# Kernel tuning notes

Hardware: AMD Instinct MI355X
Metric: run time of the kernel (lower is better)

Reference implementation:

```python
import jax, jax.numpy as jnp
import numpy as np

B, S, D, F, E = 4, 1024, 768, 3072, 8
TOP_K = 2


def setup_inputs() -> dict:
    key = jax.random.key(0)
    k0, k1, k2, k3 = jax.random.split(key, 4)
    x = jax.random.normal(k0, (B, S, D), dtype=jnp.float32)
    w_router = jax.random.normal(k1, (D, E), dtype=jnp.float32) * 0.02
    w1 = jax.random.normal(k2, (E, D, F), dtype=jnp.float32) * 0.02
    b1 = jnp.zeros((E, F), dtype=jnp.float32)
    w2 = jax.random.normal(k3, (E, F, D), dtype=jnp.float32) * 0.02
    b2 = jnp.zeros((E, D), dtype=jnp.float32)
    return {"x": x, "w_router": w_router, "w1": w1, "b1": b1, "w2": w2, "b2": b2}


def reference(x, w_router, w1, b1, w2, b2):
    # Router: logits [B,S,E] -> softmax -> top-k -> renormalize
    router_logits = jnp.einsum('bsd,de->bse', x, w_router)
    router_probs = jax.nn.softmax(router_logits, axis=-1)
    top_k_probs, top_k_idx = jax.lax.top_k(router_probs, TOP_K)  # [B,S,K]
    top_k_probs = top_k_probs / (jnp.sum(top_k_probs, axis=-1, keepdims=True) + 1e-8)
    # Combine weights [B,S,E]: weight for expert e if selected, else 0.
    # (top-k indices are distinct, so summing one-hots over k is exact.)
    combine = jnp.sum(
        jax.nn.one_hot(top_k_idx, E, dtype=x.dtype) * top_k_probs[..., None], axis=-2)
    # Dense per-expert FFN over ALL tokens (faithful to the original masked-dense math).
    h = jax.nn.gelu(jnp.einsum('bsd,edf->ebsf', x, w1) + b1[:, None, None, :],
                    approximate=False)  # [E,B,S,F]
    expert_out = jnp.einsum('ebsf,efd->ebsd', h, w2) + b2[:, None, None, :]  # [E,B,S,D]
    output = jnp.einsum('ebsd,bse->bsd', expert_out, combine)
    return output
```

## Files before the change

### kernel.cpp

```cpp
#include <hip/hip_runtime.h>
#include <math.h>

typedef __bf16 bf16x8 __attribute__((ext_vector_type(8)));
typedef float f32x4 __attribute__((ext_vector_type(4)));

#define B_ 4
#define S_ 1024
#define D_ 768
#define F_ 3072
#define E_ 8
#define NTOK 4096
#define NSLOTP 9216

__device__ __forceinline__ void gload_lds16(const void* g, void* s) {
  __builtin_amdgcn_global_load_lds((const __attribute__((address_space(1))) void*)g,
                                   (__attribute__((address_space(3))) void*)s, 16, 0, 0);
}

template<int N> __device__ __forceinline__ void wait_vmcnt() {
  if constexpr (N == 0)      asm volatile("s_waitcnt vmcnt(0)" ::: "memory");
  else if constexpr (N == 6) asm volatile("s_waitcnt vmcnt(6)" ::: "memory");
  else static_assert(N == 0, "unhandled vmcnt");
}
#define BAR()    asm volatile("s_barrier" ::: "memory")
#define LGKM0()  do { asm volatile("s_waitcnt lgkmcnt(0)" ::: "memory"); \
                      __builtin_amdgcn_sched_barrier(0); } while (0)

__device__ __forceinline__ float gelu_f(float v) {
  float u = v * (0.7978845608f + 0.0356774081f * v * v);
  float t = 1.f - 2.f / (1.f + __expf(2.f * u));
  return 0.5f * v * (1.f + t);
}

__global__ __launch_bounds__(256) void k_router(const float* __restrict__ x,
    const float* __restrict__ wr, int* __restrict__ tki, float* __restrict__ tkw) {
  int wid = threadIdx.x >> 6, lane = threadIdx.x & 63;
  int t = blockIdx.x * 4 + wid;
  const float* xp = x + (size_t)t * D_;
  float pa[E_];
#pragma unroll
  for (int e = 0; e < E_; ++e) pa[e] = 0.f;
#pragma unroll
  for (int it = 0; it < D_ / 64; ++it) {
    int d = it * 64 + lane;
    float xv = xp[d];
    const float4* wp = (const float4*)(wr + (size_t)d * E_);
    float4 a = wp[0], b = wp[1];
    pa[0] += xv * a.x; pa[1] += xv * a.y; pa[2] += xv * a.z; pa[3] += xv * a.w;
    pa[4] += xv * b.x; pa[5] += xv * b.y; pa[6] += xv * b.z; pa[7] += xv * b.w;
  }
#pragma unroll
  for (int e = 0; e < E_; ++e) {
    float v = pa[e];
    for (int off = 32; off; off >>= 1) v += __shfl_xor(v, off);
    pa[e] = v;
  }
  if (lane == 0) {
    float m = pa[0];
#pragma unroll
    for (int e = 1; e < E_; ++e) m = fmaxf(m, pa[e]);
    float p[E_], s = 0.f;
#pragma unroll
    for (int e = 0; e < E_; ++e) { p[e] = expf(pa[e] - m); s += p[e]; }
#pragma unroll
    for (int e = 0; e < E_; ++e) p[e] = p[e] / s;
    int i0 = 0; float b0 = p[0];
#pragma unroll
    for (int e = 1; e < E_; ++e) if (p[e] > b0) { b0 = p[e]; i0 = e; }
    int i1 = -1; float b1v = -1.f;
#pragma unroll
    for (int e = 0; e < E_; ++e) if (e != i0 && p[e] > b1v) { b1v = p[e]; i1 = e; }
    float den = b0 + b1v + 1e-8f;
    tki[t * 2] = i0; tki[t * 2 + 1] = i1;
    tkw[t * 2] = b0 / den; tkw[t * 2 + 1] = b1v / den;
  }
}

__global__ __launch_bounds__(256) void k_route_all(const int* __restrict__ tki,
    int* __restrict__ stok, int* __restrict__ tslot, int* __restrict__ aoff) {
  __shared__ int cl[256][E_];
  __shared__ int tot[E_];
  __shared__ int aoffA[E_ + 1];
  int tid = threadIdx.x;
  for (int i = tid; i < NSLOTP; i += 256) stok[i] = -1;
#pragma unroll
  for (int e = 0; e < E_; ++e) cl[tid][e] = 0;
  int t0 = tid * (NTOK / 256);
#pragma unroll
  for (int i = 0; i < NTOK / 256; ++i) {
    cl[tid][tki[(t0 + i) * 2]]++;
    cl[tid][tki[(t0 + i) * 2 + 1]]++;
  }
  __syncthreads();
  if (tid < E_) {
    int run = 0;
    for (int i = 0; i < 256; ++i) { int v = cl[i][tid]; cl[i][tid] = run; run += v; }
    tot[tid] = run;
  }
  __syncthreads();
  if (tid == 0) {
    int a = 0; aoffA[0] = 0; aoff[0] = 0;
    for (int e = 0; e < E_; ++e) { a += ((tot[e] + 127) >> 7) << 7; aoffA[e + 1] = a; aoff[e + 1] = a; }
  }
  __syncthreads();
#pragma unroll
  for (int i = 0; i < NTOK / 256; ++i) {
    int t = t0 + i;
#pragma unroll
    for (int k = 0; k < 2; ++k) {
      int e = tki[t * 2 + k];
      int pos = aoffA[e] + cl[tid][e];
      cl[tid][e]++;
      stok[pos] = t;
      tslot[t * 2 + k] = pos;
    }
  }
}

__global__ __launch_bounds__(256) void k_gather(const float* __restrict__ x,
    const int* __restrict__ stok, __bf16* __restrict__ Xg) {
  int i8 = blockIdx.x * 256 + threadIdx.x;
  int flat = i8 * 8;
  int row = flat / D_;
  int col = flat - row * D_;
  int tok = stok[row];
  bf16x8 v;
  if (tok >= 0) {
    const float4* s = (const float4*)(x + (size_t)tok * D_ + col);
    float4 a = s[0], b = s[1];
    v[0] = (__bf16)a.x; v[1] = (__bf16)a.y; v[2] = (__bf16)a.z; v[3] = (__bf16)a.w;
    v[4] = (__bf16)b.x; v[5] = (__bf16)b.y; v[6] = (__bf16)b.z; v[7] = (__bf16)b.w;
  } else {
#pragma unroll
    for (int k = 0; k < 8; ++k) v[k] = (__bf16)0.f;
  }
  *(bf16x8*)(Xg + (size_t)flat) = v;
}

__global__ __launch_bounds__(256) void k_transpose(const float* __restrict__ in,
    __bf16* __restrict__ outp, int R, int C) {
  __shared__ float Ts[64][65];
  int e = blockIdx.z;
  int r0 = blockIdx.y * 64, c0 = blockIdx.x * 64;
  const float* ip = in + (size_t)e * R * C;
  int lr = threadIdx.x >> 4;
  int lc = (threadIdx.x & 15) * 4;
#pragma unroll
  for (int it = 0; it < 4; ++it) {
    int r = lr + it * 16;
    float4 v = *(const float4*)(ip + (size_t)(r0 + r) * C + c0 + lc);
    Ts[r][lc] = v.x; Ts[r][lc + 1] = v.y; Ts[r][lc + 2] = v.z; Ts[r][lc + 3] = v.w;
  }
  __syncthreads();
  int rr = (threadIdx.x & 7) * 8;
  int cc = threadIdx.x >> 3;
  __bf16* op = outp + (size_t)e * R * C + r0 + rr;
#pragma unroll
  for (int it = 0; it < 2; ++it) {
    int c = cc + it * 32;
    bf16x8 v;
#pragma unroll
    for (int i = 0; i < 8; ++i) v[i] = (__bf16)Ts[rr + i][c];
    *(bf16x8*)(op + (size_t)(c0 + c) * R) = v;
  }
}

__global__ __launch_bounds__(512, 1) void k_gemm1(
    const __bf16* __restrict__ A, const __bf16* __restrict__ Bt,
    const float* __restrict__ bias, const int* __restrict__ aoff,
    __bf16* __restrict__ Hout) {
  constexpr int KST = D_;
  constexpr int N = F_;
  constexpr int NK = KST / 64;
  constexpr int ASZ = 128 * 64;
  constexpr int BSZ = 256 * 64;
  constexpr int NB = N / 256, NMB = NSLOTP / 128, NWG = NB * NMB;

  __shared__ __align__(16) __bf16 Als[3 * ASZ];
  __shared__ __align__(16) __bf16 Bls[3 * BSZ];

  int bswz = (blockIdx.x & 7) * (NWG / 8) + (blockIdx.x >> 3);
  int mb = bswz % NMB, nb = bswz / NMB;
  int row0 = mb * 128;
  if (row0 >= aoff[E_]) return;
  int e = 0;
#pragma unroll
  for (int q = 0; q < E_; ++q) if (row0 >= aoff[q + 1]) e = q + 1;
  const __bf16* Bp = Bt + (size_t)e * D_ * F_;

  int tid = threadIdx.x, w = tid >> 6, l = tid & 63;
  int fr = l & 15, fg = l >> 4;
  int wr = w >> 2, wc = w & 3;

  int ur = tid >> 3;
  int us = tid & 7;
  int ukk = us >> 2, uf4 = us & 3;

  auto SA = [&](int kt, int b) {
#pragma unroll
    for (int u = 0; u < 2; ++u) {
      int r = u * 64 + ur;
      int f4s = uf4 ^ ((r >> 1) & 3);
      gload_lds16(A + (size_t)(row0 + r) * KST + kt * 64 + ukk * 32 + f4s * 8,
                  Als + b * ASZ + u * 4096 + w * 512);
    }
  };
  auto SB = [&](int kt, int b, int u0, int u1) {
    for (int u = u0; u < u1; ++u) {
      int r = u * 64 + ur;
      int f4s = uf4 ^ ((r >> 1) & 3);
      gload_lds16(Bp + (size_t)(nb * 256 + r) * KST + kt * 64 + ukk * 32 + f4s * 8,
                  Bls + b * BSZ + u * 4096 + w * 512);
    }
  };

  SA(0, 0); SB(0, 0, 0, 4);
  SA(1, 1); SB(1, 1, 0, 4);

  f32x4 acc[4][4] = {};
  for (int t = 0; t < NK; ++t) {
    int b = t % 3, bs = (t + 2) % 3;
    bool st = (t + 2) < NK;
    if (t + 1 < NK) wait_vmcnt<6>(); else wait_vmcnt<0>();
    BAR();
    __builtin_amdgcn_sched_barrier(0);
    const __bf16* Ab = Als + b * ASZ;
    const __bf16* Bb = Bls + b * BSZ;
    bf16x8 af[4][2], bf0[2][2];
#pragma unroll
    for (int i = 0; i < 4; ++i) {
      int r = wr * 64 + i * 16 + fr;
      int sw = ((r >> 1) & 3);
#pragma unroll
      for (int kk = 0; kk < 2; ++kk)
        af[i][kk] = *(const bf16x8*)(Ab + r * 64 + kk * 32 + ((fg ^ sw) << 3));
    }
#pragma unroll
    for (int j = 0; j < 2; ++j) {
      int n = wc * 64 + j * 16 + fr;
      int sw = ((n >> 1) & 3);
#pragma unroll
      for (int kk = 0; kk < 2; ++kk)
        bf0[j][kk] = *(const bf16x8*)(Bb + n * 64 + kk * 32 + ((fg ^ sw) << 3));
    }
    if (st) { SA(t + 2, bs); SB(t + 2, bs, 0, 2); }
    LGKM0();
    __builtin_amdgcn_s_setprio(1);
#pragma unroll
    for (int i = 0; i < 4; ++i)
#pragma unroll
      for (int j = 0; j < 2; ++j)
#pragma unroll
        for (int kk = 0; kk < 2; ++kk)
          acc[i][j] = __builtin_amdgcn_mfma_f32_16x16x32_bf16(af[i][kk], bf0[j][kk], acc[i][j], 0, 0, 0);
    __builtin_amdgcn_s_setprio(0);
    __builtin_amdgcn_sched_barrier(0);
    BAR();
    bf16x8 bf1[2][2];
#pragma unroll
    for (int j = 0; j < 2; ++j) {
      int n = wc * 64 + (2 + j) * 16 + fr;
      int sw = ((n >> 1) & 3);
#pragma unroll
      for (int kk = 0; kk < 2; ++kk)
        bf1[j][kk] = *(const bf16x8*)(Bb + n * 64 + kk * 32 + ((fg ^ sw) << 3));
    }
    if (st) SB(t + 2, bs, 2, 4);
    LGKM0();
    __builtin_amdgcn_s_setprio(1);
#pragma unroll
    for (int i = 0; i < 4; ++i)
#pragma unroll
      for (int j = 0; j < 2; ++j)
#pragma unroll
        for (int kk = 0; kk < 2; ++kk)
          acc[i][2 + j] = __builtin_amdgcn_mfma_f32_16x16x32_bf16(af[i][kk], bf1[j][kk], acc[i][2 + j], 0, 0, 0);
    __builtin_amdgcn_s_setprio(0);
    __builtin_amdgcn_sched_barrier(0);
  }

#pragma unroll
  for (int j = 0; j < 4; ++j) {
    int col = nb * 256 + wc * 64 + j * 16 + fr;
    float bv = bias[e * N + col];
#pragma unroll
    for (int i = 0; i < 4; ++i) {
#pragma unroll
      for (int r = 0; r < 4; ++r) {
        int row = row0 + wr * 64 + i * 16 + fg * 4 + r;
        Hout[(size_t)row * N + col] = (__bf16)gelu_f(acc[i][j][r] + bv);
      }
    }
  }
}

template<int KST, int N, int KSPLIT>
__global__ __launch_bounds__(512, 4) void k_gemm2(
    const __bf16* __restrict__ A, const __bf16* __restrict__ Bt,
    const float* __restrict__ bias, const int* __restrict__ aoff,
    float* __restrict__ E0, float* __restrict__ E1) {
  constexpr int BN = 256;
  constexpr int ASZ = 128 * 32;
  constexpr int BSZ = BN * 32;
  constexpr int NK = KST / 32 / KSPLIT;
  constexpr int NB = N / BN;
  constexpr int NMB = NSLOTP / 128;
  constexpr int NWGB = NB * NMB;
  constexpr int NWG = NWGB * KSPLIT;

  __shared__ __align__(16) __bf16 Als[2 * ASZ];
  __shared__ __align__(16) __bf16 Bls[2 * BSZ];

  int bswz = (blockIdx.x & 7) * (NWG / 8) + (blockIdx.x >> 3);
  int kh = bswz / NWGB;
  int rem = bswz % NWGB;
  int mb = rem % NMB, nb = rem / NMB;
  int row0 = mb * 128;
  if (row0 >= aoff[E_]) return;
  int e = 0;
#pragma unroll
  for (int q = 0; q < E_; ++q) if (row0 >= aoff[q + 1]) e = q + 1;
  const __bf16* Bp = Bt + (size_t)e * D_ * F_;
  int kbase = kh * (KST / KSPLIT);

  int tid = threadIdx.x, w = tid >> 6, l = tid & 63;
  int lr = l >> 2, ls = l & 3;
  int fr = l & 15, fg = l >> 4;
  int wrow = (w >> 2) * 64, wcol = (w & 3) * 64;

  auto STAGE = [&](int kt, int b) {
    int k0 = kbase + kt * 32;
    {
      int rowA = w * 16 + lr;
      int sA = ls ^ ((rowA >> 1) & 3);
      gload_lds16(A + (size_t)(row0 + rowA) * KST + k0 + sA * 8, Als + b * ASZ + w * 512);
    }
#pragma unroll
    for (int q = 0; q < 2; ++q) {
      int idx = w * 2 + q;
      int rowB = idx * 16 + lr;
      int sB = ls ^ ((rowB >> 1) & 3);
      gload_lds16(Bp + (size_t)(nb * BN + rowB) * KST + k0 + sB * 8, Bls + b * BSZ + idx * 512);
    }
  };

  f32x4 acc[4][4] = {};
  STAGE(0, 0);
  asm volatile("s_waitcnt vmcnt(0)" ::: "memory");
  __builtin_amdgcn_sched_barrier(0);
  __builtin_amdgcn_s_barrier();
  for (int t = 0; t < NK; ++t) {
    int cur = t & 1;
    if (t + 1 < NK) STAGE(t + 1, cur ^ 1);
    __builtin_amdgcn_sched_barrier(0);
    bf16x8 af[4], bfr[4];
#pragma unroll
    for (int i = 0; i < 4; ++i) {
      int rl = wrow + i * 16 + fr;
      af[i] = *(const bf16x8*)(Als + cur * ASZ + rl * 32 + ((fg ^ ((rl >> 1) & 3)) << 3));
    }
#pragma unroll
    for (int j = 0; j < 4; ++j) {
      int nl = wcol + j * 16 + fr;
      bfr[j] = *(const bf16x8*)(Bls + cur * BSZ + nl * 32 + ((fg ^ ((nl >> 1) & 3)) << 3));
    }
#pragma unroll
    for (int i = 0; i < 4; ++i)
#pragma unroll
      for (int j = 0; j < 4; ++j)
        acc[i][j] = __builtin_amdgcn_mfma_f32_16x16x32_bf16(af[i], bfr[j], acc[i][j], 0, 0, 0);
    __builtin_amdgcn_sched_barrier(0);
    asm volatile("s_waitcnt vmcnt(0)" ::: "memory");
    __builtin_amdgcn_s_barrier();
  }

  float* Ep = (kh == 0) ? E0 : E1;
#pragma unroll
  for (int j = 0; j < 4; ++j) {
    int col = nb * BN + wcol + j * 16 + fr;
    float bv = (kh == 0) ? bias[e * N + col] : 0.f;
#pragma unroll
    for (int i = 0; i < 4; ++i) {
#pragma unroll
      for (int r = 0; r < 4; ++r) {
        int row = row0 + wrow + i * 16 + fg * 4 + r;
        Ep[(size_t)row * N + col] = acc[i][j][r] + bv;
      }
    }
  }
}

__global__ __launch_bounds__(256) void k_combine(const float* __restrict__ E0,
    const float* __restrict__ E1, const int* __restrict__ tslot,
    const float* __restrict__ tkw, float* __restrict__ out) {
  int idx = blockIdx.x * 256 + threadIdx.x;
  int t = idx / (D_ / 4);
  int c4 = (idx - t * (D_ / 4)) * 4;
  int s0 = tslot[2 * t], s1 = tslot[2 * t + 1];
  float w0 = tkw[2 * t], w1 = tkw[2 * t + 1];
  float4 a = *(const float4*)(E0 + (size_t)s0 * D_ + c4);
  float4 b = *(const float4*)(E0 + (size_t)s1 * D_ + c4);
  float4 o;
  if (E1) {
    float4 a1 = *(const float4*)(E1 + (size_t)s0 * D_ + c4);
    float4 b1 = *(const float4*)(E1 + (size_t)s1 * D_ + c4);
    o.x = w0 * (a.x + a1.x) + w1 * (b.x + b1.x);
    o.y = w0 * (a.y + a1.y) + w1 * (b.y + b1.y);
    o.z = w0 * (a.z + a1.z) + w1 * (b.z + b1.z);
    o.w = w0 * (a.w + a1.w) + w1 * (b.w + b1.w);
  } else {
    o.x = w0 * a.x + w1 * b.x; o.y = w0 * a.y + w1 * b.y;
    o.z = w0 * a.z + w1 * b.z; o.w = w0 * a.w + w1 * b.w;
  }
  *(float4*)(out + (size_t)t * D_ + c4) = o;
}

extern "C" void kernel_launch(void* const* d_in, const int* in_sizes, int n_in,
                              void* d_out, int out_size, void* d_ws, size_t ws_size,
                              hipStream_t stream) {
  const float* x  = (const float*)d_in[0];
  const float* wr = (const float*)d_in[1];
  const float* w1 = (const float*)d_in[2];
  const float* b1 = (const float*)d_in[3];
  const float* w2 = (const float*)d_in[4];
  const float* b2 = (const float*)d_in[5];
  float* out = (float*)d_out;

  char* ws = (char*)d_ws;
  size_t o = 0;
  __bf16* w1t = (__bf16*)(ws + o); o += (size_t)E_ * D_ * F_ * 2;
  __bf16* Xg  = (__bf16*)(ws + o); o += (size_t)NSLOTP * D_ * 2;
  __bf16* w2t = (__bf16*)(ws + o); o += (size_t)E_ * D_ * F_ * 2;
  __bf16* H   = (__bf16*)(ws + o); o += (size_t)NSLOTP * F_ * 2;
  int*   tki  = (int*)(ws + o);   o += (size_t)NTOK * 2 * 4;
  float* tkw  = (float*)(ws + o); o += (size_t)NTOK * 2 * 4;
  int*   stok = (int*)(ws + o);   o += (size_t)NSLOTP * 4;
  int*   tslot= (int*)(ws + o);   o += (size_t)NTOK * 2 * 4;
  int*   aoff = (int*)(ws + o);   o += 64;
  float* E0   = (float*)w1t;
  float* E1   = (float*)(ws + o);
  size_t oE1  = o + (size_t)NSLOTP * D_ * 4;
  if (ws_size < o) return;
  bool split = (ws_size >= oE1);

  k_router<<<NTOK / 4, 256, 0, stream>>>(x, wr, tki, tkw);
  k_route_all<<<1, 256, 0, stream>>>(tki, stok, tslot, aoff);
  k_gather<<<(NSLOTP * D_ / 8) / 256, 256, 0, stream>>>(x, stok, Xg);
  k_transpose<<<dim3(F_ / 64, D_ / 64, E_), 256, 0, stream>>>(w1, w1t, D_, F_);
  k_transpose<<<dim3(D_ / 64, F_ / 64, E_), 256, 0, stream>>>(w2, w2t, F_, D_);
  k_gemm1<<<(F_ / 256) * (NSLOTP / 128), 512, 0, stream>>>(Xg, w1t, b1, aoff, H);
  if (split) {
    k_gemm2<F_, D_, 2><<<2 * (D_ / 256) * (NSLOTP / 128), 512, 0, stream>>>(
        H, w2t, b2, aoff, E0, E1);
    k_combine<<<NTOK * (D_ / 4) / 256, 256, 0, stream>>>(E0, E1, tslot, tkw, out);
  } else {
    k_gemm2<F_, D_, 1><<<(D_ / 256) * (NSLOTP / 128), 512, 0, stream>>>(
        H, w2t, b2, aoff, E0, nullptr);
    k_combine<<<NTOK * (D_ / 4) / 256, 256, 0, stream>>>(E0, nullptr, tslot, tkw, out);
  }
}
```

Baseline: 227.4 us.

## Enlarge gemm1 tile to 256x256 with double buffering; store expert outputs in fp16

The first expert GEMM now uses 256x256 output tiles with a two-stage LDS double buffer and an 8-way XOR swizzle. Expert segments are padded to 256 rows, so the slot buffer grows. The second GEMM writes split-K partials as fp16 instead of fp32, and the combine reads 8-wide fp16 vectors, which halves intermediate traffic. Workspace is cut by reusing one transposed-weight buffer for w1 then w2 and aliasing E0 onto Xg. The cost is extra padded rows, possibly lower occupancy from larger accumulators, and fp16 precision on partial sums.

```diff
diff --git a/kernel.cpp b/kernel.cpp
--- a/kernel.cpp
+++ b/kernel.cpp
@@ -3,6 +3,8 @@
 
 typedef __bf16 bf16x8 __attribute__((ext_vector_type(8)));
 typedef float f32x4 __attribute__((ext_vector_type(4)));
+typedef _Float16 f16;
+typedef _Float16 f16x8 __attribute__((ext_vector_type(8)));
 
 #define B_ 4
 #define S_ 1024
@@ -10,7 +12,7 @@
 #define F_ 3072
 #define E_ 8
 #define NTOK 4096
-#define NSLOTP 9216
+#define NSLOTP 10240
 
 __device__ __forceinline__ void gload_lds16(const void* g, void* s) {
   __builtin_amdgcn_global_load_lds((const __attribute__((address_space(1))) void*)g,
@@ -19,7 +21,7 @@
 
 template<int N> __device__ __forceinline__ void wait_vmcnt() {
   if constexpr (N == 0)      asm volatile("s_waitcnt vmcnt(0)" ::: "memory");
-  else if constexpr (N == 6) asm volatile("s_waitcnt vmcnt(6)" ::: "memory");
+  else if constexpr (N == 4) asm volatile("s_waitcnt vmcnt(4)" ::: "memory");
   else static_assert(N == 0, "unhandled vmcnt");
 }
 #define BAR()    asm volatile("s_barrier" ::: "memory")
@@ -100,7 +102,7 @@
   __syncthreads();
   if (tid == 0) {
     int a = 0; aoffA[0] = 0; aoff[0] = 0;
-    for (int e = 0; e < E_; ++e) { a += ((tot[e] + 127) >> 7) << 7; aoffA[e + 1] = a; aoff[e + 1] = a; }
+    for (int e = 0; e < E_; ++e) { a += ((tot[e] + 255) >> 8) << 8; aoffA[e + 1] = a; aoff[e + 1] = a; }
   }
   __syncthreads();
 #pragma unroll
@@ -165,23 +167,20 @@
   }
 }
 
-__global__ __launch_bounds__(512, 1) void k_gemm1(
-    const __bf16* __restrict__ A, const __bf16* __restrict__ Bt,
+__global__ __launch_bounds__(512, 2) void k_gemm1(
+    const __bf16* __restrict__ Ag, const __bf16* __restrict__ Bt,
     const float* __restrict__ bias, const int* __restrict__ aoff,
     __bf16* __restrict__ Hout) {
-  constexpr int KST = D_;
-  constexpr int N = F_;
-  constexpr int NK = KST / 64;
-  constexpr int ASZ = 128 * 64;
-  constexpr int BSZ = 256 * 64;
-  constexpr int NB = N / 256, NMB = NSLOTP / 128, NWG = NB * NMB;
-
-  __shared__ __align__(16) __bf16 Als[3 * ASZ];
-  __shared__ __align__(16) __bf16 Bls[3 * BSZ];
+  constexpr int KST = D_, N = F_, NK = KST / 64;
+  constexpr int BUFE = 256 * 64;
+  constexpr int NB = N / 256, NMB = NSLOTP / 256, NWG = NB * NMB;
+
+  __shared__ __align__(16) __bf16 Als[2 * BUFE];
+  __shared__ __align__(16) __bf16 Bls[2 * BUFE];
 
   int bswz = (blockIdx.x & 7) * (NWG / 8) + (blockIdx.x >> 3);
   int mb = bswz % NMB, nb = bswz / NMB;
-  int row0 = mb * 128;
+  int row0 = mb * 256;
   if (row0 >= aoff[E_]) return;
   int e = 0;
 #pragma unroll
@@ -191,59 +190,56 @@
   int tid = threadIdx.x, w = tid >> 6, l = tid & 63;
   int fr = l & 15, fg = l >> 4;
   int wr = w >> 2, wc = w & 3;
-
-  int ur = tid >> 3;
-  int us = tid & 7;
-  int ukk = us >> 2, uf4 = us & 3;
-
-  auto SA = [&](int kt, int b) {
-#pragma unroll
-    for (int u = 0; u < 2; ++u) {
-      int r = u * 64 + ur;
-      int f4s = uf4 ^ ((r >> 1) & 3);
-      gload_lds16(A + (size_t)(row0 + r) * KST + kt * 64 + ukk * 32 + f4s * 8,
-                  Als + b * ASZ + u * 4096 + w * 512);
+  int ur = tid >> 3, us = tid & 7;
+  int src_sl = us ^ (ur & 7);
+  int r7 = fr & 7;
+
+  auto SH_A = [&](int kt, int b, int m) {
+#pragma unroll
+    for (int q = 0; q < 2; ++q) {
+      int grow = q * 128 + m * 64 + ur;
+      gload_lds16(Ag + (size_t)(row0 + grow) * KST + kt * 64 + src_sl * 8,
+                  Als + b * BUFE + (m * 128 + q * 64) * 64 + tid * 8);
     }
   };
-  auto SB = [&](int kt, int b, int u0, int u1) {
-    for (int u = u0; u < u1; ++u) {
-      int r = u * 64 + ur;
-      int f4s = uf4 ^ ((r >> 1) & 3);
-      gload_lds16(Bp + (size_t)(nb * 256 + r) * KST + kt * 64 + ukk * 32 + f4s * 8,
-                  Bls + b * BSZ + u * 4096 + w * 512);
+  auto SH_B = [&](int kt, int b, int n) {
+#pragma unroll
+    for (int q = 0; q < 2; ++q) {
+      int grow = ((q << 1) + (ur >> 5)) * 64 + n * 32 + (ur & 31);
+      gload_lds16(Bp + (size_t)(nb * 256 + grow) * KST + kt * 64 + src_sl * 8,
+                  Bls + b * BUFE + (n * 128 + q * 64) * 64 + tid * 8);
     }
   };
 
-  SA(0, 0); SB(0, 0, 0, 4);
-  SA(1, 1); SB(1, 1, 0, 4);
-
-  f32x4 acc[4][4] = {};
-  for (int t = 0; t < NK; ++t) {
-    int b = t % 3, bs = (t + 2) % 3;
-    bool st = (t + 2) < NK;
-    if (t + 1 < NK) wait_vmcnt<6>(); else wait_vmcnt<0>();
-    BAR();
-    __builtin_amdgcn_sched_barrier(0);
-    const __bf16* Ab = Als + b * ASZ;
-    const __bf16* Bb = Bls + b * BSZ;
-    bf16x8 af[4][2], bf0[2][2];
+  SH_A(0, 0, 0); SH_B(0, 0, 0); SH_A(0, 0, 1); SH_B(0, 0, 1);
+  SH_A(1, 1, 0); SH_B(1, 1, 0);
+  wait_vmcnt<4>();
+  __builtin_amdgcn_sched_barrier(0);
+  BAR();
+
+  f32x4 acc[8][4] = {};
+  bf16x8 af[4][2], bfr[2][2][2];
+  for (int kt = 0; kt < NK; ++kt) {
+    int b = kt & 1;
+    const __bf16* Ab = Als + b * BUFE;
+    const __bf16* Bb = Bls + b * BUFE;
+    bool s1 = (kt + 1) < NK, s2 = (kt + 2) < NK;
+    int b1 = (kt + 1) & 1, b2 = kt & 1;
+    if (s1) SH_A(kt + 1, b1, 1);
 #pragma unroll
     for (int i = 0; i < 4; ++i) {
-      int r = wr * 64 + i * 16 + fr;
-      int sw = ((r >> 1) & 3);
+      int p = wr * 64 + i * 16 + fr;
 #pragma unroll
       for (int kk = 0; kk < 2; ++kk)
-        af[i][kk] = *(const bf16x8*)(Ab + r * 64 + kk * 32 + ((fg ^ sw) << 3));
+        af[i][kk] = *(const bf16x8*)(Ab + p * 64 + (((kk * 4 + fg) ^ r7) << 3));
     }
 #pragma unroll
     for (int j = 0; j < 2; ++j) {
-      int n = wc * 64 + j * 16 + fr;
-      int sw = ((n >> 1) & 3);
+      int p = wc * 32 + j * 16 + fr;
 #pragma unroll
       for (int kk = 0; kk < 2; ++kk)
-        bf0[j][kk] = *(const bf16x8*)(Bb + n * 64 + kk * 32 + ((fg ^ sw) << 3));
-    }
-    if (st) { SA(t + 2, bs); SB(t + 2, bs, 0, 2); }
+        bfr[0][j][kk] = *(const bf16x8*)(Bb + p * 64 + (((kk * 4 + fg) ^ r7) << 3));
+    }
     LGKM0();
     __builtin_amdgcn_s_setprio(1);
 #pragma unroll
@@ -252,20 +248,18 @@
       for (int j = 0; j < 2; ++j)
 #pragma unroll
         for (int kk = 0; kk < 2; ++kk)
-          acc[i][j] = __builtin_amdgcn_mfma_f32_16x16x32_bf16(af[i][kk], bf0[j][kk], acc[i][j], 0, 0, 0);
+          acc[i][j] = __builtin_amdgcn_mfma_f32_16x16x32_bf16(af[i][kk], bfr[0][j][kk], acc[i][j], 0, 0, 0);
     __builtin_amdgcn_s_setprio(0);
     __builtin_amdgcn_sched_barrier(0);
     BAR();
-    bf16x8 bf1[2][2];
+    if (s1) SH_B(kt + 1, b1, 1);
 #pragma unroll
     for (int j = 0; j < 2; ++j) {
-      int n = wc * 64 + (2 + j) * 16 + fr;
-      int sw = ((n >> 1) & 3);
+      int p = 128 + wc * 32 + j * 16 + fr;
 #pragma unroll
       for (int kk = 0; kk < 2; ++kk)
-        bf1[j][kk] = *(const bf16x8*)(Bb + n * 64 + kk * 32 + ((fg ^ sw) << 3));
-    }
-    if (st) SB(t + 2, bs, 2, 4);
+        bfr[1][j][kk] = *(const bf16x8*)(Bb + p * 64 + (((kk * 4 + fg) ^ r7) << 3));
+    }
     LGKM0();
     __builtin_amdgcn_s_setprio(1);
 #pragma unroll
@@ -274,21 +268,56 @@
       for (int j = 0; j < 2; ++j)
 #pragma unroll
         for (int kk = 0; kk < 2; ++kk)
-          acc[i][2 + j] = __builtin_amdgcn_mfma_f32_16x16x32_bf16(af[i][kk], bf1[j][kk], acc[i][2 + j], 0, 0, 0);
+          acc[i][2 + j] = __builtin_amdgcn_mfma_f32_16x16x32_bf16(af[i][kk], bfr[1][j][kk], acc[i][2 + j], 0, 0, 0);
     __builtin_amdgcn_s_setprio(0);
     __builtin_amdgcn_sched_barrier(0);
-  }
-
-#pragma unroll
-  for (int j = 0; j < 4; ++j) {
-    int col = nb * 256 + wc * 64 + j * 16 + fr;
+    BAR();
+    if (s2) SH_A(kt + 2, b2, 0);
+#pragma unroll
+    for (int i = 0; i < 4; ++i) {
+      int p = 128 + wr * 64 + i * 16 + fr;
+#pragma unroll
+      for (int kk = 0; kk < 2; ++kk)
+        af[i][kk] = *(const bf16x8*)(Ab + p * 64 + (((kk * 4 + fg) ^ r7) << 3));
+    }
+    LGKM0();
+    __builtin_amdgcn_s_setprio(1);
+#pragma unroll
+    for (int i = 0; i < 4; ++i)
+#pragma unroll
+      for (int j = 0; j < 2; ++j)
+#pragma unroll
+        for (int kk = 0; kk < 2; ++kk)
+          acc[4 + i][j] = __builtin_amdgcn_mfma_f32_16x16x32_bf16(af[i][kk], bfr[0][j][kk], acc[4 + i][j], 0, 0, 0);
+    __builtin_amdgcn_s_setprio(0);
+    __builtin_amdgcn_sched_barrier(0);
+    BAR();
+    if (s2) SH_B(kt + 2, b2, 0);
+    __builtin_amdgcn_s_setprio(1);
+#pragma unroll
+    for (int i = 0; i < 4; ++i)
+#pragma unroll
+      for (int j = 0; j < 2; ++j)
+#pragma unroll
+        for (int kk = 0; kk < 2; ++kk)
+          acc[4 + i][2 + j] = __builtin_amdgcn_mfma_f32_16x16x32_bf16(af[i][kk], bfr[1][j][kk], acc[4 + i][2 + j], 0, 0, 0);
+    __builtin_amdgcn_s_setprio(0);
+    __builtin_amdgcn_sched_barrier(0);
+    if (s2)      wait_vmcnt<4>();
+    else if (s1) wait_vmcnt<0>();
+    BAR();
+  }
+
+#pragma unroll
+  for (int NN = 0; NN < 4; ++NN) {
+    int col = nb * 256 + wc * 64 + NN * 16 + fr;
     float bv = bias[e * N + col];
 #pragma unroll
-    for (int i = 0; i < 4; ++i) {
+    for (int M = 0; M < 8; ++M) {
 #pragma unroll
       for (int r = 0; r < 4; ++r) {
-        int row = row0 + wr * 64 + i * 16 + fg * 4 + r;
-        Hout[(size_t)row * N + col] = (__bf16)gelu_f(acc[i][j][r] + bv);
+        int row = row0 + wr * 128 + M * 16 + fg * 4 + r;
+        Hout[(size_t)row * N + col] = (__bf16)gelu_f(acc[M][NN][r] + bv);
       }
     }
   }
@@ -298,7 +327,7 @@
 __global__ __launch_bounds__(512, 4) void k_gemm2(
     const __bf16* __restrict__ A, const __bf16* __restrict__ Bt,
     const float* __restrict__ bias, const int* __restrict__ aoff,
-    float* __restrict__ E0, float* __restrict__ E1) {
+    f16* __restrict__ E0, f16* __restrict__ E1) {
   constexpr int BN = 256;
   constexpr int ASZ = 128 * 32;
   constexpr int BSZ = BN * 32;
@@ -374,7 +403,7 @@
     __builtin_amdgcn_s_barrier();
   }
 
-  float* Ep = (kh == 0) ? E0 : E1;
+  f16* Ep = (kh == 0) ? E0 : E1;
 #pragma unroll
   for (int j = 0; j < 4; ++j) {
     int col = nb * BN + wcol + j * 16 + fr;
@@ -384,35 +413,30 @@
 #pragma unroll
       for (int r = 0; r < 4; ++r) {
         int row = row0 + wrow + i * 16 + fg * 4 + r;
-        Ep[(size_t)row * N + col] = acc[i][j][r] + bv;
+        Ep[(size_t)row * N + col] = (f16)(acc[i][j][r] + bv);
       }
     }
   }
 }
 
-__global__ __launch_bounds__(256) void k_combine(const float* __restrict__ E0,
-    const float* __restrict__ E1, const int* __restrict__ tslot,
+__global__ __launch_bounds__(256) void k_combine(const f16* __restrict__ E0,
+    const f16* __restrict__ E1, const int* __restrict__ tslot,
     const float* __restrict__ tkw, float* __restrict__ out) {
   int idx = blockIdx.x * 256 + threadIdx.x;
-  int t = idx / (D_ / 4);
-  int c4 = (idx - t * (D_ / 4)) * 4;
+  int t = idx / (D_ / 8);
+  int c8 = (idx - t * (D_ / 8)) * 8;
   int s0 = tslot[2 * t], s1 = tslot[2 * t + 1];
   float w0 = tkw[2 * t], w1 = tkw[2 * t + 1];
-  float4 a = *(const float4*)(E0 + (size_t)s0 * D_ + c4);
-  float4 b = *(const float4*)(E0 + (size_t)s1 * D_ + c4);
-  float4 o;
-  if (E1) {
-    float4 a1 = *(const float4*)(E1 + (size_t)s0 * D_ + c4);
-    float4 b1 = *(const float4*)(E1 + (size_t)s1 * D_ + c4);
-    o.x = w0 * (a.x + a1.x) + w1 * (b.x + b1.x);
-    o.y = w0 * (a.y + a1.y) + w1 * (b.y + b1.y);
-    o.z = w0 * (a.z + a1.z) + w1 * (b.z + b1.z);
-    o.w = w0 * (a.w + a1.w) + w1 * (b.w + b1.w);
-  } else {
-    o.x = w0 * a.x + w1 * b.x; o.y = w0 * a.y + w1 * b.y;
-    o.z = w0 * a.z + w1 * b.z; o.w = w0 * a.w + w1 * b.w;
-  }
-  *(float4*)(out + (size_t)t * D_ + c4) = o;
+  f16x8 a0 = *(const f16x8*)(E0 + (size_t)s0 * D_ + c8);
+  f16x8 b0 = *(const f16x8*)(E0 + (size_t)s1 * D_ + c8);
+  f16x8 a1 = *(const f16x8*)(E1 + (size_t)s0 * D_ + c8);
+  f16x8 b1 = *(const f16x8*)(E1 + (size_t)s1 * D_ + c8);
+  float o[8];
+#pragma unroll
+  for (int k = 0; k < 8; ++k)
+    o[k] = w0 * ((float)a0[k] + (float)a1[k]) + w1 * ((float)b0[k] + (float)b1[k]);
+  *(float4*)(out + (size_t)t * D_ + c8)     = *(float4*)&o[0];
+  *(float4*)(out + (size_t)t * D_ + c8 + 4) = *(float4*)&o[4];
 }
 
 extern "C" void kernel_launch(void* const* d_in, const int* in_sizes, int n_in,
@@ -428,34 +452,25 @@
 
   char* ws = (char*)d_ws;
   size_t o = 0;
-  __bf16* w1t = (__bf16*)(ws + o); o += (size_t)E_ * D_ * F_ * 2;
+  __bf16* wt  = (__bf16*)(ws + o); o += (size_t)E_ * D_ * F_ * 2;
   __bf16* Xg  = (__bf16*)(ws + o); o += (size_t)NSLOTP * D_ * 2;
-  __bf16* w2t = (__bf16*)(ws + o); o += (size_t)E_ * D_ * F_ * 2;
   __bf16* H   = (__bf16*)(ws + o); o += (size_t)NSLOTP * F_ * 2;
+  f16*   E1p  = (f16*)(ws + o);   o += (size_t)NSLOTP * D_ * 2;
   int*   tki  = (int*)(ws + o);   o += (size_t)NTOK * 2 * 4;
   float* tkw  = (float*)(ws + o); o += (size_t)NTOK * 2 * 4;
   int*   stok = (int*)(ws + o);   o += (size_t)NSLOTP * 4;
   int*   tslot= (int*)(ws + o);   o += (size_t)NTOK * 2 * 4;
   int*   aoff = (int*)(ws + o);   o += 64;
-  float* E0   = (float*)w1t;
-  float* E1   = (float*)(ws + o);
-  size_t oE1  = o + (size_t)NSLOTP * D_ * 4;
+  f16*   E0p  = (f16*)Xg;
   if (ws_size < o) return;
-  bool split = (ws_size >= oE1);
 
   k_router<<<NTOK / 4, 256, 0, stream>>>(x, wr, tki, tkw);
   k_route_all<<<1, 256, 0, stream>>>(tki, stok, tslot, aoff);
   k_gather<<<(NSLOTP * D_ / 8) / 256, 256, 0, stream>>>(x, stok, Xg);
-  k_transpose<<<dim3(F_ / 64, D_ / 64, E_), 256, 0, stream>>>(w1, w1t, D_, F_);
-  k_transpose<<<dim3(D_ / 64, F_ / 64, E_), 256, 0, stream>>>(w2, w2t, F_, D_);
-  k_gemm1<<<(F_ / 256) * (NSLOTP / 128), 512, 0, stream>>>(Xg, w1t, b1, aoff, H);
-  if (split) {
-    k_gemm2<F_, D_, 2><<<2 * (D_ / 256) * (NSLOTP / 128), 512, 0, stream>>>(
-        H, w2t, b2, aoff, E0, E1);
-    k_combine<<<NTOK * (D_ / 4) / 256, 256, 0, stream>>>(E0, E1, tslot, tkw, out);
-  } else {
-    k_gemm2<F_, D_, 1><<<(D_ / 256) * (NSLOTP / 128), 512, 0, stream>>>(
-        H, w2t, b2, aoff, E0, nullptr);
-    k_combine<<<NTOK * (D_ / 4) / 256, 256, 0, stream>>>(E0, nullptr, tslot, tkw, out);
-  }
-}
+  k_transpose<<<dim3(F_ / 64, D_ / 64, E_), 256, 0, stream>>>(w1, wt, D_, F_);
+  k_gemm1<<<(F_ / 256) * (NSLOTP / 256), 512, 0, stream>>>(Xg, wt, b1, aoff, H);
+  k_transpose<<<dim3(D_ / 64, F_ / 64, E_), 256, 0, stream>>>(w2, wt, F_, D_);
+  k_gemm2<F_, D_, 2><<<2 * (D_ / 256) * (NSLOTP / 128), 512, 0, stream>>>(
+      H, wt, b2, aoff, E0p, E1p);
+  k_combine<<<NTOK * (D_ / 8) / 256, 256, 0, stream>>>(E0p, E1p, tslot, tkw, out);
+}
```

Result: faster. 214.2 us (-5.8%).
